# Kernel tuning notes

Measured on AMD Instinct MI355X. Metric: run time of the kernel, lower is better.

Reference implementation:

```python
import jax, jax.numpy as jnp
import numpy as np

# dims
B, T, H = 4, 2048, 768
HEADS, D = 4, 768          # GATConv(out_channels=768, heads=4, concat=False)
L = 3                      # num_layers
WIN = 2
K = 2 * WIN + 1
EPS = 1e-5
NEG_SLOPE = 0.2            # PyG GATConv leaky_relu slope


def setup_inputs() -> dict:
    key = jax.random.key(0)
    ks = jax.random.split(key, 4)
    s = 1.0 / np.sqrt(H)
    x = jax.random.normal(ks[0], (B, T, H), jnp.float32)
    W = jax.random.normal(ks[1], (L, H, HEADS, D), jnp.float32) * s   # lin weights per layer
    a_src = jax.random.normal(ks[2], (L, HEADS, D), jnp.float32) * s  # att_src
    a_dst = jax.random.normal(ks[3], (L, HEADS, D), jnp.float32) * s  # att_dst
    bias = jnp.zeros((L, D), jnp.float32)                             # GATConv bias (concat=False -> [D])
    gamma = jnp.ones((L, H), jnp.float32)                             # LayerNorm weight
    beta = jnp.zeros((L, H), jnp.float32)                             # LayerNorm bias
    return {"x": x, "W": W, "a_src": a_src, "a_dst": a_dst,
            "bias": bias, "gamma": gamma, "beta": beta}


def _layernorm(z, g, b):
    m = jnp.mean(z, axis=-1, keepdims=True)
    v = jnp.mean((z - m) ** 2, axis=-1, keepdims=True)
    return (z - m) * jax.lax.rsqrt(v + EPS) * g + b


def _gat_layer(x, Wl, asrc_w, adst_w, bias_l, idx, mask):
    # x: [B,T,H]; banded GAT with neighborhoods idx: [T,K] (clipped), mask: [T,K]
    h = jnp.einsum('bti,ihd->bthd', x, Wl)                 # [B,T,heads,D]
    asrc = jnp.einsum('bthd,hd->bth', h, asrc_w)           # per-source-node score term
    adst = jnp.einsum('bthd,hd->bth', h, adst_w)           # per-target-node score term
    h_nb = h[:, idx]                                       # [B,T,K,heads,D] gathered neighbors j
    score = jax.nn.leaky_relu(asrc[:, idx] + adst[:, :, None, :], NEG_SLOPE)  # [B,T,K,heads]
    score = jnp.where(mask[None, :, :, None], score, -jnp.inf)
    attn = jax.nn.softmax(score, axis=2)                   # softmax over incoming edges per target
    out = jnp.einsum('btkh,btkhd->bthd', attn, h_nb)       # weighted aggregation
    return out.mean(axis=2) + bias_l                       # concat=False -> mean over heads


def reference(x, W, a_src, a_dst, bias, gamma, beta):
    # banded neighborhood indices (window edges both directions + self-loop from PyG default)
    offs = jnp.arange(-WIN, WIN + 1)
    idx = jnp.arange(T)[:, None] + offs[None, :]           # [T,K]
    mask = (idx >= 0) & (idx < T)
    idx = jnp.clip(idx, 0, T - 1)
    for l in range(L):
        res = x
        y = _gat_layer(x, W[l], a_src[l], a_dst[l], bias[l], idx, mask)
        x = _layernorm(y + res, gamma[l], beta[l])         # dropout = identity in eval
    return x
```

## Files before the change

### kernel.cpp

```cpp
#include <hip/hip_runtime.h>
#include <stdint.h>

#define TT 2048
#define BB 4
#define HH 768
#define NHEADS 4
#define DD 768
#define NN 3072
#define LL 3
#define BT 8192
#define KNB 5
#define NBLK 12

typedef __bf16 bf16x8 __attribute__((ext_vector_type(8)));
typedef float f32x4 __attribute__((ext_vector_type(4)));

__device__ __forceinline__ unsigned short f2bf(float f){
  union { float f; unsigned u; } v; v.f = f;
  unsigned u = v.u;
  return (unsigned short)((u + 0x7FFFu + ((u >> 16) & 1u)) >> 16);
}
__device__ __forceinline__ float bf2f(unsigned short h){
  union { unsigned u; float f; } v; v.u = ((unsigned)h) << 16;
  return v.f;
}
__device__ __forceinline__ void gload16(const unsigned short* g, unsigned short* l){
  __builtin_amdgcn_global_load_lds((const __attribute__((address_space(1))) void*)g,
                                   (__attribute__((address_space(3))) void*)l, 16, 0, 0);
}

__global__ void wt_kernel(const float* __restrict__ W, unsigned short* __restrict__ Wt){
  __shared__ float tile[32][33];
  int l = blockIdx.z;
  int n0 = blockIdx.x * 32, k0 = blockIdx.y * 32;
  int tx = threadIdx.x, ty = threadIdx.y;
  const float* Wl = W + (size_t)l * HH * NN;
  for (int r = 0; r < 4; r++)
    tile[ty + r*8][tx] = Wl[(size_t)(k0 + ty + r*8) * NN + n0 + tx];
  __syncthreads();
  unsigned short* Wtl = Wt + (size_t)l * NN * HH;
  for (int r = 0; r < 4; r++){
    int n = n0 + ty + r*8;
    Wtl[(size_t)n * HH + k0 + tx] = f2bf(tile[tx][ty + r*8]);
  }
}

__global__ void xconv_kernel(const float* __restrict__ x, unsigned short* __restrict__ xb){
  int i = blockIdx.x * blockDim.x + threadIdx.x;
  float4 v = ((const float4*)x)[i];
  ushort4 o;
  o.x = f2bf(v.x); o.y = f2bf(v.y); o.z = f2bf(v.z); o.w = f2bf(v.w);
  *(ushort4*)(xb + (size_t)i * 4) = o;
}

#define BM 128
#define BN 128
#define BK 64

__global__ __launch_bounds__(256, 3) void gemm_kernel(
    const unsigned short* __restrict__ xb,
    const unsigned short* __restrict__ wt,
    unsigned short* __restrict__ hout,
    const float* __restrict__ a_srcl,
    const float* __restrict__ a_dstl,
    float* __restrict__ psrc,
    float* __restrict__ pdst){
  __shared__ __align__(16) unsigned short xs[BM][BK];
  __shared__ __align__(16) unsigned short wsd[BN][BK];
  int id = blockIdx.x;
  int xcd = id & 7;
  int s = id >> 3;
  int bn_i = s / 8;
  int bm_i = (s & 7) + xcd * 8;
  int bm = bm_i * BM;
  int bn = bn_i * BN;
  int tid = threadIdx.x;
  int wave = tid >> 6, lane = tid & 63;
  int m16 = lane & 15, q = lane >> 4;
  int wm = (wave >> 1) * 64, wn = (wave & 1) * 64;
  int r8 = lane >> 3, c8 = lane & 7;
  int cg = (c8 ^ r8) * 8;
  const unsigned short* ga[4]; const unsigned short* gb[4];
  unsigned short* la[4]; unsigned short* lb[4];
  #pragma unroll
  for (int ss = 0; ss < 4; ss++){
    int row = wave * 32 + ss * 8;
    ga[ss] = xb + (size_t)(bm + row + r8) * HH + cg;
    gb[ss] = wt + (size_t)(bn + row + r8) * HH + cg;
    la[ss] = &xs[row][0];
    lb[ss] = &wsd[row][0];
  }
  int rd0 = ((0 + q) ^ (m16 & 7)) * 8;
  int rd1 = ((4 + q) ^ (m16 & 7)) * 8;
  f32x4 acc[4][4] = {};
  for (int k0 = 0; k0 < HH; k0 += BK){
    #pragma unroll
    for (int ss = 0; ss < 4; ss++){
      gload16(ga[ss] + k0, la[ss]);
      gload16(gb[ss] + k0, lb[ss]);
    }
    __syncthreads();
    bf16x8 af[4], bfr[4];
    for (int i = 0; i < 4; i++)
      af[i] = __builtin_bit_cast(bf16x8, *(const uint4*)(&xs[wm + i*16 + m16][rd0]));
    for (int j = 0; j < 4; j++)
      bfr[j] = __builtin_bit_cast(bf16x8, *(const uint4*)(&wsd[wn + j*16 + m16][rd0]));
    for (int i = 0; i < 4; i++)
      for (int j = 0; j < 4; j++)
        acc[i][j] = __builtin_amdgcn_mfma_f32_16x16x32_bf16(af[i], bfr[j], acc[i][j], 0, 0, 0);
    for (int i = 0; i < 4; i++)
      af[i] = __builtin_bit_cast(bf16x8, *(const uint4*)(&xs[wm + i*16 + m16][rd1]));
    for (int j = 0; j < 4; j++)
      bfr[j] = __builtin_bit_cast(bf16x8, *(const uint4*)(&wsd[wn + j*16 + m16][rd1]));
    for (int i = 0; i < 4; i++)
      for (int j = 0; j < 4; j++)
        acc[i][j] = __builtin_amdgcn_mfma_f32_16x16x32_bf16(af[i], bfr[j], acc[i][j], 0, 0, 0);
    __syncthreads();
  }
  for (int i = 0; i < 4; i++){
    int row0 = bm + wm + i*16 + q*4;
    for (int j = 0; j < 4; j++){
      int col = bn + wn + j*16 + m16;
      unsigned short* hp = hout + (size_t)row0 * NN + col;
      hp[0]            = f2bf(acc[i][j][0]);
      hp[NN]           = f2bf(acc[i][j][1]);
      hp[2*(size_t)NN] = f2bf(acc[i][j][2]);
      hp[3*(size_t)NN] = f2bf(acc[i][j][3]);
    }
  }
  int col0 = bn + wn;
  int head = col0 / DD;
  int blk  = (col0 % DD) >> 6;
  float wsrc[4], wdstw[4];
  for (int j = 0; j < 4; j++){
    int n = col0 + j*16 + m16;
    wsrc[j]  = a_srcl[n];
    wdstw[j] = a_dstl[n];
  }
  for (int i = 0; i < 4; i++){
    for (int reg = 0; reg < 4; reg++){
      float ss = 0.f, dd = 0.f;
      for (int j = 0; j < 4; j++){
        float v = acc[i][j][reg];
        ss += v * wsrc[j];
        dd += v * wdstw[j];
      }
      ss += __shfl_xor(ss, 1, 64); dd += __shfl_xor(dd, 1, 64);
      ss += __shfl_xor(ss, 2, 64); dd += __shfl_xor(dd, 2, 64);
      ss += __shfl_xor(ss, 4, 64); dd += __shfl_xor(dd, 4, 64);
      ss += __shfl_xor(ss, 8, 64); dd += __shfl_xor(dd, 8, 64);
      if (m16 == 0){
        int row = bm + wm + i*16 + q*4 + reg;
        size_t slot = (size_t)row * (NHEADS * NBLK) + head * NBLK + blk;
        psrc[slot] = ss;
        pdst[slot] = dd;
      }
    }
  }
}

__global__ __launch_bounds__(512) void attn_ln_kernel(const unsigned short* __restrict__ h,
    const float* __restrict__ psrc, const float* __restrict__ pdst,
    const float* __restrict__ xin_f32,
    const unsigned short* __restrict__ xin_bf,
    const float* __restrict__ bias_l,
    const float* __restrict__ gamma_l, const float* __restrict__ beta_l,
    float* __restrict__ x_out, unsigned short* __restrict__ xb_next,
    int write_f32){
  int bid = blockIdx.x;
  int grp = ((bid & 7) << 7) | (bid >> 3);
  int wave = threadIdx.x >> 6, lane = threadIdx.x & 63;
  int token = grp * 8 + wave;
  int t = token & (TT - 1);
  int bseq = token >> 11;
  int e8 = lane * 8;
  int e4 = 512 + lane * 4;

  float red = 0.f;
  if (lane < 24){
    const float* p;
    if (lane < 20){
      int k = lane >> 2, hd = lane & 3;
      int row = min(max(t - 2 + k, 0), TT - 1);
      p = psrc + ((size_t)(bseq * TT + row) * NHEADS + hd) * NBLK;
    } else {
      int hd = lane - 20;
      p = pdst + ((size_t)(bseq * TT + t) * NHEADS + hd) * NBLK;
    }
    float4 a = *(const float4*)(p);
    float4 b = *(const float4*)(p + 4);
    float4 d = *(const float4*)(p + 8);
    red = a.x+a.y+a.z+a.w + b.x+b.y+b.z+b.w + d.x+d.y+d.z+d.w;
  }

  const unsigned short* hrow = h + (size_t)(bseq * TT) * NN;
  float y[12] = {};
  #pragma unroll
  for (int hd = 0; hd < NHEADS; hd++){
    float ad = __shfl(red, 20 + hd, 64);
    float sc[KNB];
    float mx = -3.0e38f;
    #pragma unroll
    for (int k = 0; k < KNB; k++){
      int tn = t + k - 2;
      if (tn >= 0 && tn < TT){
        float s = __shfl(red, k * 4 + hd, 64) + ad;
        s = s > 0.f ? s : 0.2f * s;
        sc[k] = s; mx = fmaxf(mx, s);
      } else sc[k] = -3.0e38f;
    }
    float den = 0.f;
    #pragma unroll
    for (int k = 0; k < KNB; k++){
      float e = (sc[k] > -1.0e38f) ? __expf(sc[k] - mx) : 0.f;
      sc[k] = e; den += e;
    }
    float inv = 0.25f / den;
    #pragma unroll
    for (int k = 0; k < KNB; k++){
      int g = t + k - 2;
      g = min(max(g, 0), TT - 1);
      const unsigned short* hp = hrow + (size_t)g * NN + hd * DD;
      float a = sc[k] * inv;
      uint4 u = *(const uint4*)(hp + e8);
      uint2 v = *(const uint2*)(hp + e4);
      const unsigned short* us = (const unsigned short*)&u;
      const unsigned short* vs = (const unsigned short*)&v;
      #pragma unroll
      for (int e = 0; e < 8; e++) y[e]   += a * bf2f(us[e]);
      #pragma unroll
      for (int e = 0; e < 4; e++) y[8+e] += a * bf2f(vs[e]);
    }
  }

  float xr[12], bb[12];
  if (xin_f32){
    const float* xp = xin_f32 + (size_t)token * HH;
    *(float4*)&xr[0] = *(const float4*)(xp + e8);
    *(float4*)&xr[4] = *(const float4*)(xp + e8 + 4);
    *(float4*)&xr[8] = *(const float4*)(xp + e4);
  } else {
    const unsigned short* xp = xin_bf + (size_t)token * HH;
    uint4 u = *(const uint4*)(xp + e8);
    uint2 v = *(const uint2*)(xp + e4);
    const unsigned short* us = (const unsigned short*)&u;
    const unsigned short* vs = (const unsigned short*)&v;
    #pragma unroll
    for (int e = 0; e < 8; e++) xr[e]   = bf2f(us[e]);
    #pragma unroll
    for (int e = 0; e < 4; e++) xr[8+e] = bf2f(vs[e]);
  }
  { const float* p = bias_l;
    *(float4*)&bb[0] = *(const float4*)(p + e8);
    *(float4*)&bb[4] = *(const float4*)(p + e8 + 4);
    *(float4*)&bb[8] = *(const float4*)(p + e4); }
  float s = 0.f, sq = 0.f;
  #pragma unroll
  for (int e = 0; e < 12; e++){
    float zz = y[e] + bb[e] + xr[e];
    y[e] = zz; s += zz; sq += zz * zz;
  }
  #pragma unroll
  for (int off = 32; off > 0; off >>= 1){
    s  += __shfl_xor(s, off, 64);
    sq += __shfl_xor(sq, off, 64);
  }
  float mean = s * (1.f / HH);
  float var = sq * (1.f / HH) - mean * mean;
  float rstd = rsqrtf(var + 1e-5f);

  float gr[12], br[12];
  { const float* p = gamma_l;
    *(float4*)&gr[0] = *(const float4*)(p + e8);
    *(float4*)&gr[4] = *(const float4*)(p + e8 + 4);
    *(float4*)&gr[8] = *(const float4*)(p + e4); }
  { const float* p = beta_l;
    *(float4*)&br[0] = *(const float4*)(p + e8);
    *(float4*)&br[4] = *(const float4*)(p + e8 + 4);
    *(float4*)&br[8] = *(const float4*)(p + e4); }

  float o[12];
  #pragma unroll
  for (int e = 0; e < 12; e++)
    o[e] = (y[e] - mean) * rstd * gr[e] + br[e];

  if (write_f32){
    float* xo = x_out + (size_t)token * HH;
    *(float4*)(xo + e8)     = *(float4*)&o[0];
    *(float4*)(xo + e8 + 4) = *(float4*)&o[4];
    *(float4*)(xo + e4)     = *(float4*)&o[8];
  } else {
    unsigned short* xo = xb_next + (size_t)token * HH;
    unsigned short o16[8];
    #pragma unroll
    for (int e = 0; e < 8; e++) o16[e] = f2bf(o[e]);
    *(uint4*)(xo + e8) = *(uint4*)&o16[0];
    ushort4 o4;
    o4.x = f2bf(o[8]); o4.y = f2bf(o[9]); o4.z = f2bf(o[10]); o4.w = f2bf(o[11]);
    *(ushort4*)(xo + e4) = o4;
  }
}

extern "C" void kernel_launch(void* const* d_in, const int* in_sizes, int n_in,
                              void* d_out, int out_size, void* d_ws, size_t ws_size,
                              hipStream_t stream) {
  const float* x     = (const float*)d_in[0];
  const float* W     = (const float*)d_in[1];
  const float* a_src = (const float*)d_in[2];
  const float* a_dst = (const float*)d_in[3];
  const float* bias  = (const float*)d_in[4];
  const float* gamma = (const float*)d_in[5];
  const float* beta  = (const float*)d_in[6];
  float* out = (float*)d_out;

  char* ws = (char*)d_ws;
  size_t off = 0;
  auto alloc = [&](size_t bytes)->char*{
    char* p = ws + off;
    off = (off + bytes + 255) & ~(size_t)255;
    return p;
  };
  unsigned short* wt   = (unsigned short*)alloc((size_t)LL * NN * HH * 2);
  unsigned short* xb   = (unsigned short*)alloc((size_t)BT * HH * 2);
  unsigned short* hbuf = (unsigned short*)alloc((size_t)BT * NN * 2);
  float* psrc  = (float*)alloc((size_t)BT * NHEADS * NBLK * 4);
  float* pdst  = (float*)alloc((size_t)BT * NHEADS * NBLK * 4);

  wt_kernel<<<dim3(NN/32, HH/32, LL), dim3(32, 8), 0, stream>>>(W, wt);
  xconv_kernel<<<(BT * HH / 4) / 256, 256, 0, stream>>>(x, xb);

  for (int l = 0; l < LL; l++){
    gemm_kernel<<<(NN / BN) * (BT / BM), 256, 0, stream>>>(
        xb, wt + (size_t)l * NN * HH, hbuf,
        a_src + (size_t)l * NHEADS * DD, a_dst + (size_t)l * NHEADS * DD,
        psrc, pdst);
    attn_ln_kernel<<<BT / 8, 512, 0, stream>>>(hbuf, psrc, pdst,
        (l == 0) ? x : nullptr, xb,
        bias + (size_t)l * DD, gamma + (size_t)l * HH, beta + (size_t)l * HH,
        out, xb, (l == LL - 1) ? 1 : 0);
  }
}
```

Baseline: 317.7 us.

## Double-buffer LDS tiles in GEMM to overlap global loads with MFMA

Turns the GEMM k-loop into a two-stage pipeline. LDS tiles for x and W are double-buffered, and the next tile's async global-to-LDS loads are issued before computing on the current one. Explicit vmcnt waits and raw barriers replace the per-iteration __syncthreads pair. This doubles LDS use and lowers launch-bounds occupancy from 3 to 2 blocks per CU, in exchange for hiding global load latency behind matrix-core work.

```diff
diff --git a/kernel.cpp b/kernel.cpp
--- a/kernel.cpp
+++ b/kernel.cpp
@@ -11,6 +11,7 @@
 #define BT 8192
 #define KNB 5
 #define NBLK 12
+#define NKT 12
 
 typedef __bf16 bf16x8 __attribute__((ext_vector_type(8)));
 typedef float f32x4 __attribute__((ext_vector_type(4)));
@@ -57,7 +58,7 @@
 #define BN 128
 #define BK 64
 
-__global__ __launch_bounds__(256, 3) void gemm_kernel(
+__global__ __launch_bounds__(256, 2) void gemm_kernel(
     const unsigned short* __restrict__ xb,
     const unsigned short* __restrict__ wt,
     unsigned short* __restrict__ hout,
@@ -65,8 +66,8 @@
     const float* __restrict__ a_dstl,
     float* __restrict__ psrc,
     float* __restrict__ pdst){
-  __shared__ __align__(16) unsigned short xs[BM][BK];
-  __shared__ __align__(16) unsigned short wsd[BN][BK];
+  __shared__ __align__(16) unsigned short xs[2][BM][BK];
+  __shared__ __align__(16) unsigned short wsd[2][BN][BK];
   int id = blockIdx.x;
   int xcd = id & 7;
   int s = id >> 3;
@@ -87,36 +88,60 @@
     int row = wave * 32 + ss * 8;
     ga[ss] = xb + (size_t)(bm + row + r8) * HH + cg;
     gb[ss] = wt + (size_t)(bn + row + r8) * HH + cg;
-    la[ss] = &xs[row][0];
-    lb[ss] = &wsd[row][0];
+    la[ss] = &xs[0][row][0];
+    lb[ss] = &wsd[0][row][0];
   }
   int rd0 = ((0 + q) ^ (m16 & 7)) * 8;
   int rd1 = ((4 + q) ^ (m16 & 7)) * 8;
   f32x4 acc[4][4] = {};
-  for (int k0 = 0; k0 < HH; k0 += BK){
-    #pragma unroll
-    for (int ss = 0; ss < 4; ss++){
-      gload16(ga[ss] + k0, la[ss]);
-      gload16(gb[ss] + k0, lb[ss]);
-    }
-    __syncthreads();
+
+  #pragma unroll
+  for (int ss = 0; ss < 4; ss++){
+    gload16(ga[ss], la[ss]);
+    gload16(gb[ss], lb[ss]);
+  }
+
+  #pragma unroll 2
+  for (int kt = 0; kt < NKT; kt++){
+    int cur = kt & 1, nxt = cur ^ 1;
+    if (kt < NKT - 1){
+      int k0n = (kt + 1) * BK;
+      #pragma unroll
+      for (int ss = 0; ss < 4; ss++){
+        gload16(ga[ss] + k0n, la[ss] + nxt * (BM * BK));
+        gload16(gb[ss] + k0n, lb[ss] + nxt * (BN * BK));
+      }
+      asm volatile("s_waitcnt vmcnt(8)" ::: "memory");
+    } else {
+      asm volatile("s_waitcnt vmcnt(0)" ::: "memory");
+    }
+    __builtin_amdgcn_s_barrier();
     bf16x8 af[4], bfr[4];
+    #pragma unroll
     for (int i = 0; i < 4; i++)
-      af[i] = __builtin_bit_cast(bf16x8, *(const uint4*)(&xs[wm + i*16 + m16][rd0]));
+      af[i] = __builtin_bit_cast(bf16x8, *(const uint4*)(&xs[cur][wm + i*16 + m16][rd0]));
+    #pragma unroll
     for (int j = 0; j < 4; j++)
-      bfr[j] = __builtin_bit_cast(bf16x8, *(const uint4*)(&wsd[wn + j*16 + m16][rd0]));
+      bfr[j] = __builtin_bit_cast(bf16x8, *(const uint4*)(&wsd[cur][wn + j*16 + m16][rd0]));
+    #pragma unroll
     for (int i = 0; i < 4; i++)
+      #pragma unroll
       for (int j = 0; j < 4; j++)
         acc[i][j] = __builtin_amdgcn_mfma_f32_16x16x32_bf16(af[i], bfr[j], acc[i][j], 0, 0, 0);
+    #pragma unroll
     for (int i = 0; i < 4; i++)
-      af[i] = __builtin_bit_cast(bf16x8, *(const uint4*)(&xs[wm + i*16 + m16][rd1]));
+      af[i] = __builtin_bit_cast(bf16x8, *(const uint4*)(&xs[cur][wm + i*16 + m16][rd1]));
+    #pragma unroll
     for (int j = 0; j < 4; j++)
-      bfr[j] = __builtin_bit_cast(bf16x8, *(const uint4*)(&wsd[wn + j*16 + m16][rd1]));
+      bfr[j] = __builtin_bit_cast(bf16x8, *(const uint4*)(&wsd[cur][wn + j*16 + m16][rd1]));
+    #pragma unroll
     for (int i = 0; i < 4; i++)
+      #pragma unroll
       for (int j = 0; j < 4; j++)
         acc[i][j] = __builtin_amdgcn_mfma_f32_16x16x32_bf16(af[i], bfr[j], acc[i][j], 0, 0, 0);
-    __syncthreads();
-  }
+    __builtin_amdgcn_s_barrier();
+  }
+
   for (int i = 0; i < 4; i++){
     int row0 = bm + wm + i*16 + q*4;
     for (int j = 0; j < 4; j++){
```

Measured after the change: 343.6 us. +8.1%, slower.
